# Optimization experiments

Hardware: AMD Instinct MI355X
Metric: run time of the kernel (lower is better)

## Reference

```python
import jax, jax.numpy as jnp
import numpy as np

B, T, D = 4, 2048, 2048
H = 16
HD = D // H  # head_dim = 128


def setup_inputs() -> dict:
    key = jax.random.key(0)
    ks = jax.random.split(key, 10)
    s = 0.02
    return {
        "x": jax.random.normal(ks[0], (B, T, D), dtype=jnp.float32),
        "Wq": jax.random.normal(ks[1], (D, D), dtype=jnp.float32) * s,
        "bq": jnp.zeros((D,), dtype=jnp.float32),
        "Wk": jax.random.normal(ks[2], (D, D), dtype=jnp.float32) * s,
        "bk": jnp.zeros((D,), dtype=jnp.float32),
        "Wv": jax.random.normal(ks[3], (D, D), dtype=jnp.float32) * s,
        "bv": jnp.zeros((D,), dtype=jnp.float32),
        "Wo": jax.random.normal(ks[4], (D, D), dtype=jnp.float32) * s,
        "bo": jnp.zeros((D,), dtype=jnp.float32),
    }


def reference(x, Wq, bq, Wk, bk, Wv, bv, Wo, bo):
    b, t, _ = x.shape
    # projections (nn.Linear: x @ W.T + b); split heads -> (b, h, t, hd)
    def split_heads(y):
        return y.reshape(b, t, H, HD).transpose(0, 2, 1, 3)

    q = split_heads(x @ Wq.T + bq)
    k = split_heads(x @ Wk.T + bk)
    v = split_heads(x @ Wv.T + bv)

    scale = 1.0 / jnp.sqrt(jnp.float32(HD))
    scores = jnp.einsum("bhqd,bhkd->bhqk", q, k) * scale  # (b,h,t,t)
    causal = jnp.triu(jnp.ones((t, t), dtype=bool), k=1)
    scores = jnp.where(causal, -jnp.inf, scores)
    attn = jax.nn.softmax(scores, axis=-1)
    # dropout p=0.0 -> identity
    ctx = jnp.einsum("bhqk,bhkd->bhqd", attn, v)  # (b,h,t,hd)
    ctx = ctx.transpose(0, 2, 1, 3).reshape(b, t, D)
    return ctx @ Wo.T + bo
```

## Files before the change

kernel.cpp:

```cpp
#include <hip/hip_runtime.h>
#include <hip/hip_bf16.h>

typedef __attribute__((ext_vector_type(8))) __bf16 bf16x8;
typedef __attribute__((ext_vector_type(4))) __bf16 bf16x4;
typedef __attribute__((ext_vector_type(4))) short s16x4;
typedef __attribute__((ext_vector_type(4))) float f32x4;
typedef unsigned int u32;

#define LOG2E 1.4426950408889634f

__device__ __forceinline__ void gload_lds16(const void* g, void* l) {
  __builtin_amdgcn_global_load_lds(
      (const __attribute__((address_space(1))) u32*)g,
      (__attribute__((address_space(3))) u32*)l, 16, 0, 0);
}

__global__ __launch_bounds__(256)
void cvt_f32_bf16(const float* __restrict__ src, __hip_bfloat16* __restrict__ dst, int n4) {
  int i = blockIdx.x * blockDim.x + threadIdx.x;
  if (i < n4) {
    float4 v = ((const float4*)src)[i];
    union { unsigned long long u; __hip_bfloat16 h[4]; } o;
    o.h[0] = __float2bfloat16(v.x);
    o.h[1] = __float2bfloat16(v.y);
    o.h[2] = __float2bfloat16(v.z);
    o.h[3] = __float2bfloat16(v.w);
    ((unsigned long long*)dst)[i] = o.u;
  }
}

__global__ __launch_bounds__(256)
void cvt_all(const float* __restrict__ x,
             const float* __restrict__ w0, const float* __restrict__ w1,
             const float* __restrict__ w2, const float* __restrict__ w3,
             __hip_bfloat16* __restrict__ xb,
             __hip_bfloat16* __restrict__ b0, __hip_bfloat16* __restrict__ b1,
             __hip_bfloat16* __restrict__ b2, __hip_bfloat16* __restrict__ b3,
             int n4x, int n4wlog)
{
  int i = blockIdx.x * blockDim.x + threadIdx.x;
  const float* src; __hip_bfloat16* dst; int off;
  if (i < n4x) { src = x; dst = xb; off = i; }
  else {
    int j = i - n4x;
    int which = j >> n4wlog;
    off = j & ((1 << n4wlog) - 1);
    src = which == 0 ? w0 : which == 1 ? w1 : which == 2 ? w2 : w3;
    dst = which == 0 ? b0 : which == 1 ? b1 : which == 2 ? b2 : b3;
  }
  float4 v = ((const float4*)src)[off];
  union { unsigned long long u; __hip_bfloat16 h[4]; } o;
  o.h[0] = __float2bfloat16(v.x);
  o.h[1] = __float2bfloat16(v.y);
  o.h[2] = __float2bfloat16(v.z);
  o.h[3] = __float2bfloat16(v.w);
  ((unsigned long long*)dst)[off] = o.u;
}

#define VMW(N) asm volatile("s_waitcnt vmcnt(" #N ")" ::: "memory")

#define GPHASE(P, MH, NH, RDA, RDB, ISSUE, WAITC, LGHINT)                      \
  {                                                                            \
    if (RDA) {                                                                 \
      _Pragma("unroll")                                                        \
      for (int i = 0; i < 4; ++i) {                                            \
        const char* pa = Ab + (((MH) * 128 + wr * 64 + i * 16 + l15) << 7);    \
        afr[i][0] = *(const bf16x8*)(pa + ph0);                                \
        afr[i][1] = *(const bf16x8*)(pa + ph1);                                \
      }                                                                        \
    }                                                                          \
    if (RDB) {                                                                 \
      _Pragma("unroll")                                                        \
      for (int j = 0; j < 2; ++j) {                                            \
        const char* pb = Bb + (((NH) * 128 + wc * 32 + j * 16 + l15) << 7);    \
        bfr[j][0] = *(const bf16x8*)(pb + ph0);                                \
        bfr[j][1] = *(const bf16x8*)(pb + ph1);                                \
      }                                                                        \
    }                                                                          \
    ISSUE;                                                                     \
    WAITC;                                                                     \
    LGHINT;                                                                    \
    __builtin_amdgcn_s_barrier();                                              \
    asm volatile("s_waitcnt lgkmcnt(0)" ::: "memory");                         \
    __builtin_amdgcn_sched_barrier(0);                                         \
    __builtin_amdgcn_s_setprio(1);                                             \
    _Pragma("unroll")                                                          \
    for (int ks = 0; ks < 2; ++ks)                                             \
      _Pragma("unroll")                                                        \
      for (int i = 0; i < 4; ++i)                                              \
        _Pragma("unroll")                                                      \
        for (int j = 0; j < 2; ++j)                                            \
          acc[P][i][j] = __builtin_amdgcn_mfma_f32_16x16x32_bf16(              \
              afr[i][ks], bfr[j][ks], acc[P][i][j], 0, 0, 0);                  \
    __builtin_amdgcn_s_setprio(0);                                             \
    __builtin_amdgcn_s_barrier();                                              \
  }

template<int MODE>
__global__ __launch_bounds__(512, 2)
void gemm256(const __hip_bfloat16* __restrict__ A,
             const __hip_bfloat16* __restrict__ W,
             const float* __restrict__ bias,
             __hip_bfloat16* __restrict__ C,
             float* __restrict__ Cf,
             int M, int N, int K, float oscale)
{
  __shared__ __align__(16) __hip_bfloat16 SH[2][32768];

  const int tid = threadIdx.x;
  const int lane = tid & 63;
  const int w = tid >> 6;
  const int wr = w >> 2, wc = w & 3;
  const int quad = lane >> 4, l15 = lane & 15;

  const int nb = N >> 8;
  const int swz = (blockIdx.x & 7) * ((int)gridDim.x >> 3) + ((int)blockIdx.x >> 3);
  const int m0 = (swz / nb) << 8;
  const int n0 = (swz % nb) << 8;

  const int NT = K >> 6;

  const int r0 = tid >> 3;
  const int kb = ((tid & 7) ^ (r0 & 7)) << 3;
  const __hip_bfloat16* Ag = A + (size_t)(m0 + r0) * K + kb;
  const __hip_bfloat16* Wg = W + (size_t)(n0 + r0) * K + kb;

  const int ph0 = (quad ^ (l15 & 7)) << 4;
  const int ph1 = ((4 + quad) ^ (l15 & 7)) << 4;

  f32x4 acc[4][4][2] = {};
  bf16x8 afr[4][2], bfr[2][2];

  auto issueA = [&](int t2, int mh) {
    if (t2 < NT) {
      const __hip_bfloat16* g = Ag + (size_t)(mh * 128) * K + (t2 << 6);
      char* l = (char*)SH[t2 & 1] + mh * 16384 + (tid << 4);
      gload_lds16(g, l);
      gload_lds16(g + (size_t)64 * K, l + 8192);
    }
  };
  auto issueB = [&](int t2, int nh) {
    if (t2 < NT) {
      const __hip_bfloat16* g = Wg + (size_t)(nh * 128) * K + (t2 << 6);
      char* l = (char*)SH[t2 & 1] + 32768 + nh * 16384 + (tid << 4);
      gload_lds16(g, l);
      gload_lds16(g + (size_t)64 * K, l + 8192);
    }
  };

  issueA(0, 0); issueB(0, 0); issueA(0, 1); issueB(0, 1);
  VMW(4);
  __builtin_amdgcn_s_barrier();

  for (int t = 0; t < NT; ++t) {
    const char* Ab = (const char*)SH[t & 1];
    const char* Bb = Ab + 32768;
    const bool more = (t + 1 < NT);

    GPHASE(0, 0, 0, true, true, issueA(t + 1, 0),
           if (more) { VMW(4); } else { VMW(2); },
           asm volatile("s_waitcnt lgkmcnt(8)" ::: "memory"));
    GPHASE(1, 1, 0, true, false, issueB(t + 1, 0),
           if (more) { VMW(4); } else { VMW(0); }, );
    GPHASE(2, 1, 1, false, true, issueA(t + 1, 1), , );
    GPHASE(3, 0, 1, true, false, issueB(t + 1, 1),
           if (more) { VMW(4); }, );
  }

#pragma unroll
  for (int p = 0; p < 4; ++p) {
    const int mh = (p == 1 || p == 2) ? 1 : 0;
    const int nh = (p >= 2) ? 1 : 0;
#pragma unroll
    for (int i = 0; i < 4; ++i) {
      int mbase = m0 + mh * 128 + wr * 64 + i * 16 + quad * 4;
#pragma unroll
      for (int j = 0; j < 2; ++j) {
        int n = n0 + nh * 128 + wc * 32 + j * 16 + l15;
        float bv = bias[n];
#pragma unroll
        for (int r = 0; r < 4; ++r) {
          int mm = mbase + r;
          float v = (acc[p][i][j][r] + bv) * oscale;
          if (MODE == 0) {
            C[(size_t)mm * N + n] = __float2bfloat16(v);
          } else if (MODE == 1) {
            int b = mm >> 11, tt = mm & 2047;
            C[((size_t)(b * 2048 + n)) * 2048 + tt] = __float2bfloat16(v);
          } else {
            Cf[(size_t)mm * N + n] = v;
          }
        }
      }
    }
  }
}

__global__ __launch_bounds__(256, 2)
void attn_fwd(const __hip_bfloat16* __restrict__ Q,
              const __hip_bfloat16* __restrict__ K,
              const __hip_bfloat16* __restrict__ Vt,
              __hip_bfloat16* __restrict__ ctx)
{
  __shared__ __align__(16) __hip_bfloat16 KVl[2][16384];

  const int tid = threadIdx.x;
  const int lane = tid & 63;
  const int w = tid >> 6;
  const int quad = lane >> 4, l15 = lane & 15;
  const int bid = blockIdx.x;
  const int qi = 15 - (bid >> 6);
  const int bh = bid & 63;
  const int b = bh >> 4, h = bh & 15;
  const int q0 = qi * 128;

  bf16x8 qf[2][4];
  for (int sub = 0; sub < 2; ++sub) {
    const __hip_bfloat16* qp =
        Q + ((size_t)(b * 2048 + q0 + sub * 64 + w * 16 + l15)) * 2048 + h * 128 + quad * 8;
    for (int ks = 0; ks < 4; ++ks) qf[sub][ks] = *(const bf16x8*)(qp + ks * 32);
  }

  int krow[4], kcol[4], vrow[4], vcol[4], soff[4];
  for (int p = 0; p < 4; ++p) {
    int off = (tid + p * 256) * 16;
    soff[p] = off;
    int r1 = off >> 8;
    int pc1 = (off >> 4) & 15;
    krow[p] = r1; kcol[p] = ((pc1 & 8) | ((pc1 & 7) ^ (r1 & 7))) * 8;
    int r2 = off >> 7;
    int pc2 = (off >> 4) & 7;
    vrow[p] = r2; vcol[p] = (pc2 ^ (r2 & 7)) * 8;
  }

  f32x4 o[2][8] = {};
  float lsum[2] = {0.f, 0.f};
  const int base0 = q0 + w * 16;
  const int base1 = q0 + 64 + w * 16;

  const int ktmax = (q0 + 127) >> 6;

  for (int p = 0; p < 4; ++p)
    gload_lds16(K + ((size_t)(b * 2048 + krow[p])) * 2048 + h * 128 + kcol[p],
                (char*)&KVl[0][0] + soff[p]);
  for (int p = 0; p < 4; ++p)
    gload_lds16(Vt + ((size_t)(b * 2048 + h * 128 + vrow[p])) * 2048 + vcol[p],
                (char*)&KVl[0][8192] + soff[p]);
  __syncthreads();

  for (int kt = 0; kt <= ktmax; ++kt) {
    const int cur = kt & 1;
    const int kbase = kt * 64;
    if (kt < ktmax) {
      const int nbase = kbase + 64;
      for (int p = 0; p < 4; ++p)
        gload_lds16(K + ((size_t)(b * 2048 + nbase + krow[p])) * 2048 + h * 128 + kcol[p],
                    (char*)&KVl[1 - cur][0] + soff[p]);
      for (int p = 0; p < 4; ++p)
        gload_lds16(Vt + ((size_t)(b * 2048 + h * 128 + vrow[p])) * 2048 + nbase + vcol[p],
                    (char*)&KVl[1 - cur][8192] + soff[p]);
    }

    const char* Kl = (const char*)&KVl[cur][0];
    const char* Vl = (const char*)&KVl[cur][8192];

    const bool act0 = kbase <= base0 + 15;
    const bool act1 = kbase <= base1 + 15;

    f32x4 s[2][4] = {};
    for (int ct = 0; ct < 4; ++ct) {
      int row = ct * 16 + l15;
      for (int ks = 0; ks < 4; ++ks) {
        int c = ks * 4 + quad;
        int ph = (c & 8) | ((c & 7) ^ (row & 7));
        bf16x8 kf = *(const bf16x8*)(Kl + row * 256 + ph * 16);
        if (act0) s[0][ct] = __builtin_amdgcn_mfma_f32_16x16x32_bf16(kf, qf[0][ks], s[0][ct], 0, 0, 0);
        if (act1) s[1][ct] = __builtin_amdgcn_mfma_f32_16x16x32_bf16(kf, qf[1][ks], s[1][ct], 0, 0, 0);
      }
    }

    s16x4 pf[2][4];
    for (int sub = 0; sub < 2; ++sub) {
      if (!(sub ? act1 : act0)) continue;
      const int bs = sub ? base1 : base0;
      const bool full = (kbase + 63 <= bs);
      float lsv = lsum[sub];
      for (int ct = 0; ct < 4; ++ct) {
        bf16x4 pb;
        if (full) {
          for (int r = 0; r < 4; ++r) {
            float e = exp2f(s[sub][ct][r]);
            lsv += e; pb[r] = (__bf16)e;
          }
        } else {
          int diff = (bs + l15) - (kbase + ct * 16 + quad * 4);
          for (int r = 0; r < 4; ++r) {
            float e = (r <= diff) ? exp2f(s[sub][ct][r]) : 0.f;
            lsv += e; pb[r] = (__bf16)e;
          }
        }
        pf[sub][ct] = __builtin_bit_cast(s16x4, pb);
      }
      lsum[sub] = lsv;
    }

    for (int dgrp = 0; dgrp < 8; ++dgrp) {
      int row = dgrp * 16 + l15;
      for (int ct = 0; ct < 4; ++ct) {
        int c = ct * 2 + (quad >> 1);
        int ph = c ^ (row & 7);
        s16x4 vf = *(const s16x4*)(Vl + row * 128 + ph * 16 + (quad & 1) * 8);
        if (act0) o[0][dgrp] = __builtin_amdgcn_mfma_f32_16x16x16bf16_1k(vf, pf[0][ct], o[0][dgrp], 0, 0, 0);
        if (act1) o[1][dgrp] = __builtin_amdgcn_mfma_f32_16x16x16bf16_1k(vf, pf[1][ct], o[1][dgrp], 0, 0, 0);
      }
    }
    __syncthreads();
  }

  for (int sub = 0; sub < 2; ++sub) {
    float ls = lsum[sub];
    ls += __shfl_xor(ls, 16, 64);
    ls += __shfl_xor(ls, 32, 64);
    lsum[sub] = 1.0f / ls;
  }

  for (int sub = 0; sub < 2; ++sub) {
    char* rb = (char*)&KVl[0][0] + (w * 2 + sub) * 4096;
    float inv = lsum[sub];
    for (int dgrp = 0; dgrp < 8; ++dgrp) {
      for (int rp = 0; rp < 2; ++rp) {
        __hip_bfloat16 lo = __float2bfloat16(o[sub][dgrp][rp * 2] * inv);
        __hip_bfloat16 hi = __float2bfloat16(o[sub][dgrp][rp * 2 + 1] * inv);
        u32 pk = (u32)*(unsigned short*)&lo | ((u32)*(unsigned short*)&hi << 16);
        int c = dgrp * 2 + (quad >> 1);
        int cp = c ^ (l15 & 7);
        *(u32*)(rb + l15 * 256 + cp * 16 + (quad & 1) * 8 + rp * 4) = pk;
      }
    }
    int q2 = lane & 15;
    int qq = q0 + sub * 64 + w * 16 + q2;
    __hip_bfloat16* cp = ctx + ((size_t)(b * 2048 + qq)) * 2048 + h * 128;
    for (int rr = 0; rr < 4; ++rr) {
      int cl = quad + rr * 4;
      int cph = cl ^ (q2 & 7);
      uint4 val = *(const uint4*)(rb + q2 * 256 + cph * 16);
      *(uint4*)(cp + cl * 8) = val;
    }
  }
}

extern "C" void kernel_launch(void* const* d_in, const int* in_sizes, int n_in,
                              void* d_out, int out_size, void* d_ws, size_t ws_size,
                              hipStream_t stream)
{
  (void)in_sizes; (void)n_in; (void)out_size;
  const float* x  = (const float*)d_in[0];
  const float* Wq = (const float*)d_in[1];
  const float* bq = (const float*)d_in[2];
  const float* Wk = (const float*)d_in[3];
  const float* bk = (const float*)d_in[4];
  const float* Wv = (const float*)d_in[5];
  const float* bv = (const float*)d_in[6];
  const float* Wo = (const float*)d_in[7];
  const float* bo = (const float*)d_in[8];
  float* out = (float*)d_out;

  const int M = 8192, D = 2048;
  const size_t MD = (size_t)M * D, DD = (size_t)D * D;
  const int n4x = (int)(MD / 4), n4w = (int)(DD / 4);
  dim3 cb(256), bb(256), ga(1024);
  dim3 gg((M / 256) * (D / 256)), gbb(512);
  const float qscale = 0.08838834764831845f * LOG2E;

  if (ws_size >= (4 * MD + 4 * DD) * 2) {
    __hip_bfloat16* xb  = (__hip_bfloat16*)d_ws;
    __hip_bfloat16* Wqb = xb  + MD;
    __hip_bfloat16* Wkb = Wqb + DD;
    __hip_bfloat16* Wvb = Wkb + DD;
    __hip_bfloat16* Wob = Wvb + DD;
    __hip_bfloat16* Qb  = Wob + DD;
    __hip_bfloat16* Kb  = Qb  + MD;
    __hip_bfloat16* Vtb = Kb  + MD;
    __hip_bfloat16* Cx  = xb;

    int tot4 = n4x + 4 * n4w;
    hipLaunchKernelGGL(cvt_all, dim3(tot4 / 256), cb, 0, stream,
                       x, Wq, Wk, Wv, Wo, xb, Wqb, Wkb, Wvb, Wob, n4x, 20);
    hipLaunchKernelGGL((gemm256<0>), gg, gbb, 0, stream, xb, Wqb, bq, Qb, (float*)nullptr, M, D, D, qscale);
    hipLaunchKernelGGL((gemm256<0>), gg, gbb, 0, stream, xb, Wkb, bk, Kb, (float*)nullptr, M, D, D, 1.0f);
    hipLaunchKernelGGL((gemm256<1>), gg, gbb, 0, stream, xb, Wvb, bv, Vtb, (float*)nullptr, M, D, D, 1.0f);
    hipLaunchKernelGGL(attn_fwd, ga, bb, 0, stream, Qb, Kb, Vtb, Cx);
    hipLaunchKernelGGL((gemm256<2>), gg, gbb, 0, stream, Cx, Wob, bo, (__hip_bfloat16*)nullptr, out, M, D, D, 1.0f);
  } else {
    __hip_bfloat16* xb  = (__hip_bfloat16*)d_ws;
    __hip_bfloat16* Wb  = xb  + MD;
    __hip_bfloat16* Qb  = Wb  + DD;
    __hip_bfloat16* Kb  = Qb  + MD;
    __hip_bfloat16* Vtb = Kb  + MD;
    __hip_bfloat16* Cx  = xb;

    dim3 cgx((n4x + 255) / 256), cgw((n4w + 255) / 256);
    hipLaunchKernelGGL(cvt_f32_bf16, cgx, cb, 0, stream, x, xb, n4x);
    hipLaunchKernelGGL(cvt_f32_bf16, cgw, cb, 0, stream, Wq, Wb, n4w);
    hipLaunchKernelGGL((gemm256<0>), gg, gbb, 0, stream, xb, Wb, bq, Qb, (float*)nullptr, M, D, D, qscale);
    hipLaunchKernelGGL(cvt_f32_bf16, cgw, cb, 0, stream, Wk, Wb, n4w);
    hipLaunchKernelGGL((gemm256<0>), gg, gbb, 0, stream, xb, Wb, bk, Kb, (float*)nullptr, M, D, D, 1.0f);
    hipLaunchKernelGGL(cvt_f32_bf16, cgw, cb, 0, stream, Wv, Wb, n4w);
    hipLaunchKernelGGL((gemm256<1>), gg, gbb, 0, stream, xb, Wb, bv, Vtb, (float*)nullptr, M, D, D, 1.0f);
    hipLaunchKernelGGL(attn_fwd, ga, bb, 0, stream, Qb, Kb, Vtb, Cx);
    hipLaunchKernelGGL(cvt_f32_bf16, cgw, cb, 0, stream, Wo, Wb, n4w);
    hipLaunchKernelGGL((gemm256<2>), gg, gbb, 0, stream, Cx, Wb, bo, (__hip_bfloat16*)nullptr, out, M, D, D, 1.0f);
  }
}
```

Baseline: 557.8 us.

## Use 16x16x32 MFMA for PV product and reorder GEMM phase schedule

In the attention kernel, pairs of probability tiles are packed into bf16x8 operands so the P·V product uses the K=32 MFMA instead of two K=16 MFMAs, halving MFMA issue count in that loop. Inner loops are explicitly unrolled. In the projection GEMM, the order of quadrant phases and of A/B prefetch issues is changed, with the epilogue quadrant mapping updated to match, to alter register/LDS fragment reuse across phases. The V fragment is assembled from two 8-byte LDS reads, which must line up correctly with the packed P layout.

```diff
diff --git a/kernel.cpp b/kernel.cpp
--- a/kernel.cpp
+++ b/kernel.cpp
@@ -148,7 +148,7 @@
     }
   };
 
-  issueA(0, 0); issueB(0, 0); issueA(0, 1); issueB(0, 1);
+  issueA(0, 0); issueB(0, 0); issueB(0, 1); issueA(0, 1);
   VMW(4);
   __builtin_amdgcn_s_barrier();
 
@@ -160,17 +160,17 @@
     GPHASE(0, 0, 0, true, true, issueA(t + 1, 0),
            if (more) { VMW(4); } else { VMW(2); },
            asm volatile("s_waitcnt lgkmcnt(8)" ::: "memory"));
-    GPHASE(1, 1, 0, true, false, issueB(t + 1, 0),
+    GPHASE(1, 0, 1, false, true, issueB(t + 1, 0),
            if (more) { VMW(4); } else { VMW(0); }, );
-    GPHASE(2, 1, 1, false, true, issueA(t + 1, 1), , );
-    GPHASE(3, 0, 1, true, false, issueB(t + 1, 1),
+    GPHASE(2, 1, 1, true, false, issueB(t + 1, 1), , );
+    GPHASE(3, 1, 0, false, true, issueA(t + 1, 1),
            if (more) { VMW(4); }, );
   }
 
 #pragma unroll
   for (int p = 0; p < 4; ++p) {
-    const int mh = (p == 1 || p == 2) ? 1 : 0;
-    const int nh = (p >= 2) ? 1 : 0;
+    const int mh = (p >= 2) ? 1 : 0;
+    const int nh = (p == 1 || p == 2) ? 1 : 0;
 #pragma unroll
     for (int i = 0; i < 4; ++i) {
       int mbase = m0 + mh * 128 + wr * 64 + i * 16 + quad * 4;
@@ -268,8 +268,10 @@
     const bool act1 = kbase <= base1 + 15;
 
     f32x4 s[2][4] = {};
+#pragma unroll
     for (int ct = 0; ct < 4; ++ct) {
       int row = ct * 16 + l15;
+#pragma unroll
       for (int ks = 0; ks < 4; ++ks) {
         int c = ks * 4 + quad;
         int ph = (c & 8) | ((c & 7) ^ (row & 7));
@@ -279,39 +281,51 @@
       }
     }
 
-    s16x4 pf[2][4];
+    union pu { bf16x4 h[2]; bf16x8 v; };
+    pu pf8[2][2];
+#pragma unroll
     for (int sub = 0; sub < 2; ++sub) {
       if (!(sub ? act1 : act0)) continue;
       const int bs = sub ? base1 : base0;
       const bool full = (kbase + 63 <= bs);
       float lsv = lsum[sub];
+#pragma unroll
       for (int ct = 0; ct < 4; ++ct) {
         bf16x4 pb;
         if (full) {
+#pragma unroll
           for (int r = 0; r < 4; ++r) {
             float e = exp2f(s[sub][ct][r]);
             lsv += e; pb[r] = (__bf16)e;
           }
         } else {
           int diff = (bs + l15) - (kbase + ct * 16 + quad * 4);
+#pragma unroll
           for (int r = 0; r < 4; ++r) {
             float e = (r <= diff) ? exp2f(s[sub][ct][r]) : 0.f;
             lsv += e; pb[r] = (__bf16)e;
           }
         }
-        pf[sub][ct] = __builtin_bit_cast(s16x4, pb);
+        pf8[sub][ct >> 1].h[ct & 1] = pb;
       }
       lsum[sub] = lsv;
     }
 
+    const int h8 = (quad & 1) * 8;
+    const int qh = quad >> 1;
+#pragma unroll
     for (int dgrp = 0; dgrp < 8; ++dgrp) {
       int row = dgrp * 16 + l15;
-      for (int ct = 0; ct < 4; ++ct) {
-        int c = ct * 2 + (quad >> 1);
-        int ph = c ^ (row & 7);
-        s16x4 vf = *(const s16x4*)(Vl + row * 128 + ph * 16 + (quad & 1) * 8);
-        if (act0) o[0][dgrp] = __builtin_amdgcn_mfma_f32_16x16x16bf16_1k(vf, pf[0][ct], o[0][dgrp], 0, 0, 0);
-        if (act1) o[1][dgrp] = __builtin_amdgcn_mfma_f32_16x16x16bf16_1k(vf, pf[1][ct], o[1][dgrp], 0, 0, 0);
+      int rx = row & 7;
+      const char* vrow_p = Vl + row * 128;
+#pragma unroll
+      for (int c = 0; c < 2; ++c) {
+        int ch1 = 4 * c + qh;
+        union { struct { s16x4 a, b; } s; bf16x8 v; } vu;
+        vu.s.a = *(const s16x4*)(vrow_p + ((ch1 ^ rx) * 16) + h8);
+        vu.s.b = *(const s16x4*)(vrow_p + (((ch1 + 2) ^ rx) * 16) + h8);
+        if (act0) o[0][dgrp] = __builtin_amdgcn_mfma_f32_16x16x32_bf16(vu.v, pf8[0][c].v, o[0][dgrp], 0, 0, 0);
+        if (act1) o[1][dgrp] = __builtin_amdgcn_mfma_f32_16x16x32_bf16(vu.v, pf8[1][c].v, o[1][dgrp], 0, 0, 0);
       }
     }
     __syncthreads();
```

After: 533.7 us. -4.3%, faster.
